# Optimization experiments

Measured on AMD Instinct MI355X. Metric: run time of the kernel, lower is better.

The kernel has to match this reference:

```python
import jax, jax.numpy as jnp
import numpy as np

N_HEADS = 16


def setup_inputs() -> dict:
    key = jax.random.key(0)
    ks = jax.random.split(key, 4)
    B, S, D = 2, 2048, 1024
    x = jax.random.normal(ks[0], (B, S, D), dtype=jnp.float32)
    scale = 1.0 / np.sqrt(D)
    Wq = jax.random.normal(ks[1], (D, D), dtype=jnp.float32) * scale
    Wk = jax.random.normal(ks[2], (D, D), dtype=jnp.float32) * scale
    Wv = jax.random.normal(ks[3], (D, D), dtype=jnp.float32) * scale
    bq = jnp.zeros((D,), jnp.float32)
    bk = jnp.zeros((D,), jnp.float32)
    bv = jnp.zeros((D,), jnp.float32)
    return {"x": x, "Wq": Wq, "bq": bq, "Wk": Wk, "bk": bk, "Wv": Wv, "bv": bv}


def _split_heads(t, n_heads):
    B, S, D = t.shape
    return t.reshape(B, S, n_heads, D // n_heads).transpose(0, 2, 1, 3)  # [B,H,S,hd]


def reference(x, Wq, bq, Wk, bk, Wv, bv):
    H = N_HEADS
    Q = _split_heads(x @ Wq + bq, H)
    K = _split_heads(x @ Wk + bk, H)
    V = _split_heads(x @ Wv + bv, H)
    head_size = Q.shape[-1]
    scores = jnp.einsum("bhqd,bhkd->bhqk", Q, K) / jnp.sqrt(jnp.float32(head_size))
    probs = jax.nn.softmax(scores, axis=-1)  # dropout p=0.01 -> identity in eval
    out = jnp.einsum("bhqk,bhkd->bhqd", probs, V)
    B, _, S, hd = out.shape
    return out.transpose(0, 2, 1, 3).reshape(B, S, H * hd)
```

## Files before the change

kernel.cpp:

```cpp
#include <hip/hip_runtime.h>
#include <hip/hip_bf16.h>

typedef __bf16 bf16x8 __attribute__((ext_vector_type(8)));
typedef __bf16 bf16x4 __attribute__((ext_vector_type(4)));
typedef float f32x4 __attribute__((ext_vector_type(4)));

#define B_ 2
#define S_ 2048
#define D_ 1024
#define H_ 16
#define HD_ 64
#define NT_ (S_ / 64)

__device__ inline void load_lds16(const __bf16* g, __bf16* l) {
  __builtin_amdgcn_global_load_lds(
      (const __attribute__((address_space(1))) void*)g,
      (__attribute__((address_space(3))) void*)l, 16, 0, 0);
}

__global__ __launch_bounds__(256) void prep(
    const float* __restrict__ X,
    const float* __restrict__ Wq, const float* __restrict__ Wk,
    const float* __restrict__ Wv,
    __bf16* __restrict__ Xb, __bf16* __restrict__ WT)
{
  const int z = blockIdx.z, t = threadIdx.x;
  if (z == 3) {
    size_t base = ((size_t)(blockIdx.y * 16 + blockIdx.x)) * 16384 + t * 4;
#pragma unroll
    for (int i = 0; i < 16; ++i) {
      size_t idx = base + (size_t)i * 1024;
      f32x4 v = *(const f32x4*)(X + idx);
      __bf16 o[4];
#pragma unroll
      for (int j = 0; j < 4; ++j) o[j] = (__bf16)v[j];
      *(ulong1*)(Xb + idx) = *(ulong1*)o;
    }
    return;
  }
  const float* W = (z == 0) ? Wq : (z == 1) ? Wk : Wv;
  __bf16* WTz = WT + (size_t)z * D_ * D_;
  const int k0 = blockIdx.y * 64, n0 = blockIdx.x * 64;

  __shared__ __bf16 T[64 * 72];
  {
    int kl = t >> 2, cg = (t & 3) * 16;
    const float* wp = W + (size_t)(k0 + kl) * D_ + n0 + cg;
    bf16x8 a, b;
#pragma unroll
    for (int j = 0; j < 4; ++j) { a[j] = (__bf16)wp[j];     a[4 + j] = (__bf16)wp[4 + j]; }
#pragma unroll
    for (int j = 0; j < 4; ++j) { b[j] = (__bf16)wp[8 + j]; b[4 + j] = (__bf16)wp[12 + j]; }
    *(bf16x8*)(T + kl * 72 + cg) = a;
    *(bf16x8*)(T + kl * 72 + cg + 8) = b;
  }
  __syncthreads();
  {
    int nl = t >> 2, kc = (t & 3) * 16;
    bf16x8 a, b;
#pragma unroll
    for (int j = 0; j < 8; ++j) a[j] = T[(kc + j) * 72 + nl];
#pragma unroll
    for (int j = 0; j < 8; ++j) b[j] = T[(kc + 8 + j) * 72 + nl];
    __bf16* op = WTz + (size_t)(n0 + nl) * D_ + k0 + kc;
    *(bf16x8*)(op) = a;
    *(bf16x8*)(op + 8) = b;
  }
}

__global__ __launch_bounds__(256) void qkv_gemm(
    const __bf16* __restrict__ Xb, const __bf16* __restrict__ WT,
    const float* __restrict__ bq, const float* __restrict__ bk,
    const float* __restrict__ bv,
    __bf16* __restrict__ Qw, __bf16* __restrict__ Kw, __bf16* __restrict__ VTw)
{
  const int z = blockIdx.z;
  const __bf16* Wz = WT + (size_t)z * D_ * D_;
  const float* bias = (z == 0) ? bq : (z == 1) ? bk : bv;
  __bf16* outp = (z == 0) ? Qw : (z == 1) ? Kw : VTw;
  const float mult = (z == 0) ? 0.125f * 1.44269504088896f : 1.0f;

  const int tid  = threadIdx.x;
  const int wave = tid >> 6, lane = tid & 63, ln = lane & 15, quad = lane >> 4;
  const int m0 = blockIdx.y * 128, n0 = blockIdx.x * 128;
  const int wm = (wave & 1) * 64, wn = (wave >> 1) * 64;

  __shared__ __bf16 Als[128 * 32];
  __shared__ __bf16 Bls[128 * 32];

  f32x4 acc[4][4] = {};

  for (int k0 = 0; k0 < D_; k0 += 32) {
    __syncthreads();
#pragma unroll
    for (int i = 0; i < 2; ++i) {
      int cb = wave * 128 + i * 64;
      int chunk = cb + lane;
      int row = chunk >> 2, c = chunk & 3;
      int gc = c ^ (row & 3);
      load_lds16(Xb + (size_t)(m0 + row) * D_ + k0 + gc * 8, Als + cb * 8);
      load_lds16(Wz + (size_t)(n0 + row) * D_ + k0 + gc * 8, Bls + cb * 8);
    }
    __syncthreads();

    bf16x8 af[4], bfr[4];
    const int dsw = (quad ^ (ln & 3)) * 8;
#pragma unroll
    for (int mt = 0; mt < 4; ++mt)
      af[mt] = *(const bf16x8*)(Als + (wm + mt * 16 + ln) * 32 + dsw);
#pragma unroll
    for (int nt = 0; nt < 4; ++nt)
      bfr[nt] = *(const bf16x8*)(Bls + (wn + nt * 16 + ln) * 32 + dsw);
#pragma unroll
    for (int mt = 0; mt < 4; ++mt)
#pragma unroll
      for (int nt = 0; nt < 4; ++nt)
        acc[mt][nt] = __builtin_amdgcn_mfma_f32_16x16x32_bf16(af[mt], bfr[nt], acc[mt][nt], 0, 0, 0);
  }

#pragma unroll
  for (int nt = 0; nt < 4; ++nt) {
    int n_g = n0 + wn + nt * 16 + ln;
    float bv_ = bias[n_g];
#pragma unroll
    for (int mt = 0; mt < 4; ++mt) {
      if (z < 2) {
#pragma unroll
        for (int r = 0; r < 4; ++r) {
          int m_g = m0 + wm + mt * 16 + quad * 4 + r;
          outp[(size_t)m_g * D_ + n_g] = (__bf16)((acc[mt][nt][r] + bv_) * mult);
        }
      } else {
        int m_g0 = m0 + wm + mt * 16 + quad * 4;
        bf16x4 v4;
#pragma unroll
        for (int r = 0; r < 4; ++r) v4[r] = (__bf16)(acc[mt][nt][r] + bv_);
        *(bf16x4*)(outp + (size_t)(m_g0 >> 11) * D_ * S_ + (size_t)n_g * S_ + (m_g0 & (S_ - 1))) = v4;
      }
    }
  }
}

__global__ __launch_bounds__(256) void attn(
    const __bf16* __restrict__ Q, const __bf16* __restrict__ K,
    const __bf16* __restrict__ VT, float* __restrict__ out)
{
  const int tid  = threadIdx.x;
  const int wave = tid >> 6, lane = tid & 63, ln = lane & 15, quad = lane >> 4;

  const int f = blockIdx.x;
  const int xcd = f & 7, g = f >> 3;
  const int bh = ((g & 3) << 3) | xcd;
  const int qt = g >> 2;
  const int b = bh >> 4, h = bh & 15;
  const int q0 = qt * 128 + wave * 32;

  const __bf16* Qbase = Q + (size_t)(b * S_ + q0) * D_ + h * HD_;
  bf16x8 qb[2][2];
#pragma unroll
  for (int nt = 0; nt < 2; ++nt)
#pragma unroll
    for (int ks = 0; ks < 2; ++ks)
      qb[nt][ks] = *(const bf16x8*)(Qbase + (size_t)(nt * 16 + ln) * D_ + ks * 32 + quad * 8);

  const __bf16* Kh = K + (size_t)b * S_ * D_ + h * HD_;
  const __bf16* Vh = VT + (size_t)(b * D_ + h * HD_) * S_;

  __shared__ __bf16 Kls[2][64 * 64];
  __shared__ __bf16 Vls[2][80 * 64];
  __shared__ __bf16 Pls[4][32 * 64];
  __bf16* Pw = Pls[wave];

  {
    bf16x8 ones;
#pragma unroll
    for (int j = 0; j < 8; ++j) ones[j] = (__bf16)1.0f;
    int buf = tid >> 7, rr = (tid >> 3) & 15, cc = tid & 7;
    *(bf16x8*)(&Vls[buf][(64 + rr) * 64 + cc * 8]) = ones;
  }

  f32x4 acc[2][5] = {};

  const int swl = ln & 7;

  bf16x8 kreg[2], vreg[2];
#pragma unroll
  for (int i = 0; i < 2; ++i) {
    int chunk = i * 256 + tid, row = chunk >> 3, cc = chunk & 7;
    kreg[i] = *(const bf16x8*)(Kh + (size_t)row * D_ + cc * 8);
    vreg[i] = *(const bf16x8*)(Vh + (size_t)row * S_ + cc * 8);
  }

  for (int kt = 0; kt < NT_; ++kt) {
    __bf16* Kb = Kls[kt & 1];
    __bf16* Vb = Vls[kt & 1];
#pragma unroll
    for (int i = 0; i < 2; ++i) {
      int chunk = i * 256 + tid, row = chunk >> 3, cc = chunk & 7;
      int sw = (cc ^ (row & 7)) * 8;
      *(bf16x8*)(Kb + row * 64 + sw) = kreg[i];
      *(bf16x8*)(Vb + row * 64 + sw) = vreg[i];
    }
    if (kt + 1 < NT_) {
#pragma unroll
      for (int i = 0; i < 2; ++i) {
        int chunk = i * 256 + tid, row = chunk >> 3, cc = chunk & 7;
        kreg[i] = *(const bf16x8*)(Kh + (size_t)((kt + 1) * 64 + row) * D_ + cc * 8);
        vreg[i] = *(const bf16x8*)(Vh + (size_t)row * S_ + (kt + 1) * 64 + cc * 8);
      }
    }
    __syncthreads();

    f32x4 st[4][2] = {};
#pragma unroll
    for (int mt = 0; mt < 4; ++mt) {
#pragma unroll
      for (int ks = 0; ks < 2; ++ks) {
        bf16x8 ka = *(const bf16x8*)(Kb + (mt * 16 + ln) * 64 + ((ks * 4 + quad) ^ swl) * 8);
#pragma unroll
        for (int nt = 0; nt < 2; ++nt)
          st[mt][nt] = __builtin_amdgcn_mfma_f32_16x16x32_bf16(ka, qb[nt][ks], st[mt][nt], 0, 0, 0);
      }
    }

#pragma unroll
    for (int mt = 0; mt < 4; ++mt)
#pragma unroll
      for (int nt = 0; nt < 2; ++nt) {
        bf16x4 pk;
#pragma unroll
        for (int r = 0; r < 4; ++r)
          pk[r] = (__bf16)__builtin_amdgcn_exp2f(st[mt][nt][r]);
        *(bf16x4*)(Pw + (nt * 16 + ln) * 64 + ((2 * mt + (quad >> 1)) ^ swl) * 8 + (quad & 1) * 4) = pk;
      }

#pragma unroll
    for (int ks = 0; ks < 2; ++ks) {
      bf16x8 pa[2];
#pragma unroll
      for (int mt = 0; mt < 2; ++mt)
        pa[mt] = *(const bf16x8*)(Pw + (mt * 16 + ln) * 64 + ((ks * 4 + quad) ^ swl) * 8);
#pragma unroll
      for (int dt = 0; dt < 5; ++dt) {
        int vrow = (dt < 4) ? dt * 16 + ln : 64 + ln;
        bf16x8 vb = *(const bf16x8*)(Vb + vrow * 64 + ((ks * 4 + quad) ^ swl) * 8);
#pragma unroll
        for (int mt = 0; mt < 2; ++mt)
          acc[mt][dt] = __builtin_amdgcn_mfma_f32_16x16x32_bf16(pa[mt], vb, acc[mt][dt], 0, 0, 0);
      }
    }
    __syncthreads();
  }

#pragma unroll
  for (int mt = 0; mt < 2; ++mt)
#pragma unroll
    for (int r = 0; r < 4; ++r) {
      float li = 1.0f / acc[mt][4][r];
      float* op = out + (size_t)(b * S_ + q0 + mt * 16 + quad * 4 + r) * D_ + h * HD_;
#pragma unroll
      for (int dt = 0; dt < 4; ++dt)
        op[dt * 16 + ln] = acc[mt][dt][r] * li;
    }
}

extern "C" void kernel_launch(void* const* d_in, const int* in_sizes, int n_in,
                              void* d_out, int out_size, void* d_ws, size_t ws_size,
                              hipStream_t stream) {
  const float* X  = (const float*)d_in[0];
  const float* Wq = (const float*)d_in[1];
  const float* bq = (const float*)d_in[2];
  const float* Wk = (const float*)d_in[3];
  const float* bk = (const float*)d_in[4];
  const float* Wv = (const float*)d_in[5];
  const float* bv = (const float*)d_in[6];

  __bf16* Qw  = (__bf16*)d_ws;
  __bf16* Kw  = Qw  + (size_t)B_ * S_ * D_;
  __bf16* VTw = Kw  + (size_t)B_ * S_ * D_;
  __bf16* Xb  = VTw + (size_t)B_ * S_ * D_;
  __bf16* WT  = Xb  + (size_t)B_ * S_ * D_;
  float* out = (float*)d_out;

  prep<<<dim3(16, 16, 4), 256, 0, stream>>>(X, Wq, Wk, Wv, Xb, WT);
  qkv_gemm<<<dim3(8, 32, 3), 256, 0, stream>>>(Xb, WT, bq, bk, bv, Qw, Kw, VTw);
  attn<<<512, 256, 0, stream>>>(Qw, Kw, VTw, out);
}
```

Measured before the change: 166.0 us.

## Keep softmax probabilities in registers via permlane swaps instead of an LDS round-trip

The exp2 results are now rearranged into the MFMA A-operand layout entirely in registers, using v_permlane32_swap and v_permlane16_swap. This replaces writing P to a per-wave LDS buffer and reading it back. The Pls shared array goes away, which cuts LDS traffic and footprint and may allow higher occupancy. The change also drops the trailing per-iteration __syncthreads, relying on the K/V double buffering for safety, and wraps the MFMA phases in s_setprio to favour matrix issue. The risk is that the permlane sequence yields the wrong operand layout, and that removing the barrier lets waves race ahead.

```diff
diff --git a/kernel.cpp b/kernel.cpp
--- a/kernel.cpp
+++ b/kernel.cpp
@@ -4,6 +4,8 @@
 typedef __bf16 bf16x8 __attribute__((ext_vector_type(8)));
 typedef __bf16 bf16x4 __attribute__((ext_vector_type(4)));
 typedef float f32x4 __attribute__((ext_vector_type(4)));
+typedef unsigned u32x2 __attribute__((ext_vector_type(2)));
+typedef unsigned u32x4 __attribute__((ext_vector_type(4)));
 
 #define B_ 2
 #define S_ 2048
@@ -168,8 +170,6 @@
 
   __shared__ __bf16 Kls[2][64 * 64];
   __shared__ __bf16 Vls[2][80 * 64];
-  __shared__ __bf16 Pls[4][32 * 64];
-  __bf16* Pw = Pls[wave];
 
   {
     bf16x8 ones;
@@ -212,6 +212,7 @@
     __syncthreads();
 
     f32x4 st[4][2] = {};
+    __builtin_amdgcn_s_setprio(1);
 #pragma unroll
     for (int mt = 0; mt < 4; ++mt) {
 #pragma unroll
@@ -222,45 +223,55 @@
           st[mt][nt] = __builtin_amdgcn_mfma_f32_16x16x32_bf16(ka, qb[nt][ks], st[mt][nt], 0, 0, 0);
       }
     }
-
-#pragma unroll
-    for (int mt = 0; mt < 4; ++mt)
-#pragma unroll
-      for (int nt = 0; nt < 2; ++nt) {
-        bf16x4 pk;
-#pragma unroll
-        for (int r = 0; r < 4; ++r)
-          pk[r] = (__bf16)__builtin_amdgcn_exp2f(st[mt][nt][r]);
-        *(bf16x4*)(Pw + (nt * 16 + ln) * 64 + ((2 * mt + (quad >> 1)) ^ swl) * 8 + (quad & 1) * 4) = pk;
-      }
-
+    __builtin_amdgcn_s_setprio(0);
+
+    bf16x8 pa[2][2];
+#pragma unroll
+    for (int nt = 0; nt < 2; ++nt)
+#pragma unroll
+      for (int ks = 0; ks < 2; ++ks) {
+        bf16x4 p0, p1;
+#pragma unroll
+        for (int r = 0; r < 4; ++r) {
+          p0[r] = (__bf16)__builtin_amdgcn_exp2f(st[2 * ks + 0][nt][r]);
+          p1[r] = (__bf16)__builtin_amdgcn_exp2f(st[2 * ks + 1][nt][r]);
+        }
+        u32x2 d0 = __builtin_bit_cast(u32x2, p0);
+        u32x2 d1 = __builtin_bit_cast(u32x2, p1);
+        unsigned a = d0[0], bw = d0[1], c = d1[0], e = d1[1];
+        asm("v_permlane32_swap_b32 %0, %1" : "+v"(a), "+v"(c));
+        asm("v_permlane16_swap_b32 %0, %1" : "+v"(a), "+v"(c));
+        asm("v_permlane32_swap_b32 %0, %1" : "+v"(bw), "+v"(e));
+        asm("v_permlane16_swap_b32 %0, %1" : "+v"(bw), "+v"(e));
+        u32x4 w;
+        w[0] = a; w[1] = bw; w[2] = c; w[3] = e;
+        pa[nt][ks] = __builtin_bit_cast(bf16x8, w);
+      }
+
+    __builtin_amdgcn_s_setprio(1);
 #pragma unroll
     for (int ks = 0; ks < 2; ++ks) {
-      bf16x8 pa[2];
-#pragma unroll
-      for (int mt = 0; mt < 2; ++mt)
-        pa[mt] = *(const bf16x8*)(Pw + (mt * 16 + ln) * 64 + ((ks * 4 + quad) ^ swl) * 8);
 #pragma unroll
       for (int dt = 0; dt < 5; ++dt) {
         int vrow = (dt < 4) ? dt * 16 + ln : 64 + ln;
         bf16x8 vb = *(const bf16x8*)(Vb + vrow * 64 + ((ks * 4 + quad) ^ swl) * 8);
 #pragma unroll
-        for (int mt = 0; mt < 2; ++mt)
-          acc[mt][dt] = __builtin_amdgcn_mfma_f32_16x16x32_bf16(pa[mt], vb, acc[mt][dt], 0, 0, 0);
-      }
-    }
-    __syncthreads();
-  }
-
-#pragma unroll
-  for (int mt = 0; mt < 2; ++mt)
+        for (int nt = 0; nt < 2; ++nt)
+          acc[nt][dt] = __builtin_amdgcn_mfma_f32_16x16x32_bf16(pa[nt][ks], vb, acc[nt][dt], 0, 0, 0);
+      }
+    }
+    __builtin_amdgcn_s_setprio(0);
+  }
+
+#pragma unroll
+  for (int nt = 0; nt < 2; ++nt)
 #pragma unroll
     for (int r = 0; r < 4; ++r) {
-      float li = 1.0f / acc[mt][4][r];
-      float* op = out + (size_t)(b * S_ + q0 + mt * 16 + quad * 4 + r) * D_ + h * HD_;
+      float li = 1.0f / acc[nt][4][r];
+      float* op = out + (size_t)(b * S_ + q0 + nt * 16 + quad * 4 + r) * D_ + h * HD_;
 #pragma unroll
       for (int dt = 0; dt < 4; ++dt)
-        op[dt * 16 + ln] = acc[mt][dt][r] * li;
+        op[dt * 16 + ln] = acc[nt][dt][r] * li;
     }
 }
 
```

New measurement: 166.4 us. About the same (+0.3%).
